# Performance work log

Hardware: AMD Instinct MI355X
Metric: run time of the kernel (lower is better)

## Reference

```python
import jax, jax.numpy as jnp
import numpy as np

N_QUBIT = 14
N_LAYER = 16
BATCH = 512
DIM = 2 ** N_QUBIT

# wire 0 is the most-significant bit (deepquantum convention: state.reshape([2]*n), wire i = axis i)
_bits = (np.arange(DIM)[:, None] >> (N_QUBIT - 1 - np.arange(N_QUBIT))) & 1
SIGNS = jnp.asarray(2.0 * _bits - 1.0, dtype=jnp.float32)  # (DIM, n_qubit), -1 for bit=0, +1 for bit=1


def _apply_1q(state, gate, w):
    # state: (B, DIM) complex64; gate: (2,2) complex
    B = state.shape[0]
    left, right = 2 ** w, 2 ** (N_QUBIT - w - 1)
    st = state.reshape(B, left, 2, right)
    return jnp.einsum('ab,xlbr->xlar', gate, st).reshape(B, DIM)


def _cnot(state, c, t):
    # CNOT control c, target t: X on target where control bit = 1
    B = state.shape[0]
    st = state.reshape((B,) + (2,) * N_QUBIT)
    ax_c, ax_t = c + 1, t + 1
    a0 = jnp.take(st, 0, axis=ax_c)
    a1 = jnp.take(st, 1, axis=ax_c)
    a1 = jnp.flip(a1, axis=ax_t if ax_t < ax_c else ax_t - 1)  # flip size-2 axis == X gate
    return jnp.stack([a0, a1], axis=ax_c).reshape(B, DIM)


def _rz_layer(state, thetas):
    # RZ(th) = diag(e^{-i th/2}, e^{+i th/2}) on every wire -> single fused diagonal phase
    return state * jnp.exp(0.5j * (SIGNS @ thetas))


def _ry_layer(state, thetas):
    for w in range(N_QUBIT):
        c = jnp.cos(thetas[w] * 0.5)
        s = jnp.sin(thetas[w] * 0.5)
        gate = jnp.stack([jnp.stack([c, -s]), jnp.stack([s, c])]).astype(jnp.complex64)
        state = _apply_1q(state, gate, w)
    return state


def _circuit(z, theta):
    state = z.reshape(z.shape[0], DIM)
    for l in range(N_LAYER):
        state = _rz_layer(state, theta[l, 0])
        state = _ry_layer(state, theta[l, 1])
        state = _rz_layer(state, theta[l, 2])
        for w in range(N_QUBIT):  # cnot_ring
            state = _cnot(state, w, (w + 1) % N_QUBIT)
    return state


def _split(state, w):
    B = state.shape[0]
    st = state.reshape(B, 2 ** w, 2, 2 ** (N_QUBIT - w - 1))
    return st[:, :, 0, :], st[:, :, 1, :]


def _expectations(state):
    outs = []
    for w in (0, 1):  # <Z_w> = sum |psi_0|^2 - |psi_1|^2
        p0, p1 = _split(state, w)
        outs.append(jnp.sum(jnp.abs(p0) ** 2 - jnp.abs(p1) ** 2, axis=(1, 2)))
    cross0 = None
    for w in (0, 1):  # <X_w> = 2 Re sum conj(psi_0) psi_1
        p0, p1 = _split(state, w)
        cr = jnp.conj(p0) * p1
        if w == 0:
            cross0 = cr
        outs.append(2.0 * jnp.sum(jnp.real(cr), axis=(1, 2)))
    outs.append(2.0 * jnp.sum(jnp.imag(cross0), axis=(1, 2)))  # <Y_0> = 2 Im sum conj(psi_0) psi_1
    return jnp.stack(outs, axis=1).astype(jnp.float32)  # (B, 5)


def setup_inputs() -> dict:
    key = jax.random.key(0)
    k1, k2, k3, k4 = jax.random.split(key, 4)
    zr = jax.random.normal(k1, (BATCH, DIM), dtype=jnp.float32)
    zi = jax.random.normal(k2, (BATCH, DIM), dtype=jnp.float32)
    z = (zr + 1j * zi).astype(jnp.complex64)
    z = z / jnp.linalg.norm(z, axis=1, keepdims=True)  # normalized quantum states
    z = z[:, :, None]  # (B, 2^n, 1) per docstring
    theta = jax.random.normal(k3, (N_LAYER, 3, N_QUBIT), dtype=jnp.float32)
    y = jax.random.randint(k4, (BATCH,), 0, 5)
    return {"z": z, "theta": theta, "y": y}


def reference(z, theta, y):
    state = _circuit(z, theta)
    output = _expectations(state)
    logp = jax.nn.log_softmax(output, axis=1)
    loss = -jnp.mean(jnp.take_along_axis(logp, y[:, None], axis=1))
    return (loss, output)
```

## Files before the change

### kernel.cpp

```cpp
#include <hip/hip_runtime.h>
#include <hip/hip_bf16.h>

#define NQ     14
#define DIM    16384
#define NLAYER 16
#define BATCH  512
#define NT     1024

typedef float v2f __attribute__((ext_vector_type(2)));

__device__ __forceinline__ constexpr int POSB(int x){ return (x ^ ((x >> 5) & 31)) << 3; }

__device__ __forceinline__ float bf2f(unsigned int u16){
  union { unsigned int i; float f; } v; v.i = u16 << 16; return v.f;
}

__device__ __forceinline__ float thv(const void* th, int i, bool b16){
  return b16 ? bf2f(((const unsigned short*)th)[i]) : ((const float*)th)[i];
}

__device__ int srcF(int x){
  int v = x;
  #pragma unroll
  for (int k = 13; k >= 0; --k){
    int tb = 13 - ((k + 1) % 14);
    v ^= ((v >> (13 - k)) & 1) << tb;
  }
  return v;
}

__device__ __forceinline__ v2f cmul(v2f a, v2f b){
  v2f t, d;
  asm("v_pk_mul_f32 %0, %1, %2 op_sel:[0,0] op_sel_hi:[1,0]"
      : "=v"(t) : "v"(a), "v"(b));
  asm("v_pk_fma_f32 %0, %1, %2, %3 op_sel:[1,1,0] op_sel_hi:[0,1,1] neg_lo:[0,1,0]"
      : "=v"(d) : "v"(a), "v"(b), "v"(t));
  return d;
}

__device__ __forceinline__ void rot2(v2f& a0, v2f& a1, float c, float s){
  v2f c2 = (v2f){c, c}, s2 = (v2f){s, s};
  v2f t0 = a0;
  a0 = a0 * c2 - a1 * s2;
  a1 = t0 * s2 + a1 * c2;
}

__global__ __launch_bounds__(NT) __attribute__((amdgpu_waves_per_eu(4, 4)))
void qnn_circuit(const void* __restrict__ zraw,
                 const void* __restrict__ theta,
                 float* __restrict__ out)
{
  __shared__ v2f   S[DIM];
  __shared__ v2f   ph0H[128], ph0L[128], ph2H[128], ph2Lt[128];
  __shared__ float csT[28];
  __shared__ int   sHB[128], sLB[128];
  __shared__ float red[16*5];

  char* Sb = (char*)S;
  const int t = threadIdx.x;
  const int b = blockIdx.x;

  int pred = 0;
  if (t < 336){
    unsigned int w  = ((const unsigned int*)theta)[t];
    unsigned int lo = w & 0xffffu;
    unsigned int e  = (lo >> 7) & 0xffu;
    pred = (e >= 100 && e <= 140) || (lo == 0);
  }
  const bool th_b16 = (__syncthreads_count(pred) > 250);

  pred = 0;
  if (t < 256){
    unsigned int w  = ((const unsigned int*)zraw)[t];
    unsigned int lo = w & 0xffffu;
    unsigned int e  = (lo >> 7) & 0xffu;
    pred = (e >= 88 && e <= 140) || (lo == 0);
  }
  const bool z_b16 = (__syncthreads_count(pred) > 160);

  if (t < 128){ sHB[t] = POSB(srcF(t << 7)); sLB[t] = POSB(srcF(t)); }

  if (z_b16){
    const uint4* zb = (const uint4*)((const unsigned short*)zraw + (size_t)b * (DIM * 2));
    #pragma unroll 1
    for (int jj = 0; jj < 4; ++jj){
      int x4 = t + NT * jj;
      uint4 w = zb[x4];
      int xb = x4 * 4;
      *(v2f*)(Sb + POSB(xb+0)) = (v2f){bf2f(w.x & 0xffffu), bf2f(w.x >> 16)};
      *(v2f*)(Sb + POSB(xb+1)) = (v2f){bf2f(w.y & 0xffffu), bf2f(w.y >> 16)};
      *(v2f*)(Sb + POSB(xb+2)) = (v2f){bf2f(w.z & 0xffffu), bf2f(w.z >> 16)};
      *(v2f*)(Sb + POSB(xb+3)) = (v2f){bf2f(w.w & 0xffffu), bf2f(w.w >> 16)};
    }
  } else {
    const float4* zf = (const float4*)((const float*)zraw + (size_t)b * DIM);
    #pragma unroll 1
    for (int jj = 0; jj < 4; ++jj){
      int x4 = t + NT * jj;
      float4 w = zf[x4];
      int xb = x4 * 4;
      *(v2f*)(Sb + POSB(xb+0)) = (v2f){w.x, 0.f};
      *(v2f*)(Sb + POSB(xb+1)) = (v2f){w.y, 0.f};
      *(v2f*)(Sb + POSB(xb+2)) = (v2f){w.z, 0.f};
      *(v2f*)(Sb + POSB(xb+3)) = (v2f){w.w, 0.f};
    }
  }
  __syncthreads();

  const int pwb = POSB(t);
  const int hb  = t >> 7;
  const int slB = sLB[t & 127];

  const int wv  = t >> 6, L = t & 63;
  const int pbA  = POSB((wv << 10) | L);
  const int pbB1 = POSB((wv << 10) | ((L >> 2) << 6) | (L & 3));
  const int pbB2 = POSB((wv << 10) | (L << 2));
  const int hB2  = (wv << 3) | (L >> 5);
  const int rB2  = L & 31;

  for (int l = 0; l < NLAYER; ++l){
    const int thb = l * 42;

    if (t < 512){
      int grp = t >> 7, idx = t & 127;
      int tz = thb + ((grp >= 2) ? 28 : 0);
      float ph = 0.f;
      if ((grp & 1) == 0){
        #pragma unroll
        for (int w = 0; w < 7; ++w)
          ph += (((idx >> (6 - w)) & 1) ? 0.5f : -0.5f) * thv(theta, tz + w, th_b16);
      } else {
        #pragma unroll
        for (int w = 7; w < 14; ++w)
          ph += (((idx >> (13 - w)) & 1) ? 0.5f : -0.5f) * thv(theta, tz + w, th_b16);
      }
      float sn, cs; sincosf(ph, &sn, &cs);
      v2f v = (v2f){cs, sn};
      if      (grp == 0) ph0H[idx] = v;
      else if (grp == 1) ph0L[idx] = v;
      else if (grp == 2) ph2H[idx] = v;
      else               ph2Lt[((idx & 3) << 5) | (idx >> 2)] = v;
    } else if (t < 512 + 14){
      int q = t - 512;
      float sn, cs; sincosf(0.5f * thv(theta, thb + 14 + q, th_b16), &sn, &cs);
      csT[2*q] = cs; csT[2*q+1] = sn;
    }

    {
      v2f g[16];
      if (l == 0){
        #pragma unroll
        for (int j = 0; j < 16; ++j) g[j] = *(v2f*)(Sb + (pwb ^ (j << 13)));
      } else {
        #pragma unroll
        for (int j = 0; j < 16; ++j)
          g[j] = *(v2f*)(Sb + (sHB[hb + 8*j] ^ slB));
      }
      __syncthreads();

      {
        v2f cl = ph0L[t & 127];
        #pragma unroll
        for (int j = 0; j < 16; ++j)
          g[j] = cmul(g[j], cmul(ph0H[hb + 8*j], cl));
      }
      #pragma unroll
      for (int q = 0; q < 4; ++q){
        float c = csT[2*q], sn = csT[2*q+1];
        int m = 8 >> q;
        #pragma unroll
        for (int j = 0; j < 16; ++j){
          if (j & m) continue;
          rot2(g[j], g[j | m], c, sn);
        }
      }
      #pragma unroll
      for (int j = 0; j < 16; ++j) *(v2f*)(Sb + (pwb ^ (j << 13))) = g[j];
    }
    __syncthreads();

    {
      v2f h[16];
      #pragma unroll
      for (int j = 0; j < 16; ++j) h[j] = *(v2f*)(Sb + (pbA ^ ((j << 9) | (j << 4))));
      #pragma unroll
      for (int q = 0; q < 4; ++q){
        float c = csT[2*(4+q)], sn = csT[2*(4+q)+1];
        int m = 8 >> q;
        #pragma unroll
        for (int j = 0; j < 16; ++j){
          if (j & m) continue;
          rot2(h[j], h[j | m], c, sn);
        }
      }
      #pragma unroll
      for (int j = 0; j < 16; ++j) *(v2f*)(Sb + (pbA ^ ((j << 9) | (j << 4)))) = h[j];
    }
    __threadfence_block();

    {
      v2f h[16];
      #pragma unroll
      for (int j = 0; j < 16; ++j)
        h[j] = *(v2f*)(Sb + (pbB1 ^ ((j << 5) ^ ((j >> 3) << 3))));
      #pragma unroll
      for (int q = 0; q < 4; ++q){
        float c = csT[2*(8+q)], sn = csT[2*(8+q)+1];
        int m = 8 >> q;
        #pragma unroll
        for (int j = 0; j < 16; ++j){
          if (j & m) continue;
          rot2(h[j], h[j | m], c, sn);
        }
      }
      #pragma unroll
      for (int j = 0; j < 16; ++j)
        *(v2f*)(Sb + (pbB1 ^ ((j << 5) ^ ((j >> 3) << 3)))) = h[j];
    }
    __threadfence_block();

    {
      v2f h[16];
      #pragma unroll
      for (int i = 0; i < 4; ++i){
        int gb = pbB2 ^ ((i << 11) | (i << 6));
        #pragma unroll
        for (int j = 0; j < 4; ++j) h[i*4+j] = *(v2f*)(Sb + (gb ^ (j << 3)));
      }
      #pragma unroll
      for (int q = 0; q < 2; ++q){
        float c = csT[2*(12+q)], sn = csT[2*(12+q)+1];
        int m = 2 >> q;
        #pragma unroll
        for (int r = 0; r < 16; ++r){
          if ((r & 3) & m) continue;
          rot2(h[r], h[r | m], c, sn);
        }
      }
      #pragma unroll
      for (int i = 0; i < 4; ++i){
        v2f chh = ph2H[hB2 | (i << 1)];
        #pragma unroll
        for (int j = 0; j < 4; ++j)
          h[i*4+j] = cmul(h[i*4+j], cmul(chh, ph2Lt[(j << 5) | rB2]));
      }
      #pragma unroll
      for (int i = 0; i < 4; ++i){
        int gb = pbB2 ^ ((i << 11) | (i << 6));
        #pragma unroll
        for (int j = 0; j < 4; ++j) *(v2f*)(Sb + (gb ^ (j << 3))) = h[i*4+j];
      }
    }
    __syncthreads();
  }

  float z0=0.f, z1=0.f, x0s=0.f, x1s=0.f, y0s=0.f;
  {
    v2f g[16];
    #pragma unroll
    for (int j = 0; j < 16; ++j)
      g[j] = *(v2f*)(Sb + (sHB[hb + 8*j] ^ slB));

    #pragma unroll
    for (int j = 0; j < 16; ++j){
      float pw = g[j].x*g[j].x + g[j].y*g[j].y;
      z0 += (j & 8) ? -pw : pw;
      z1 += (j & 4) ? -pw : pw;
    }
    #pragma unroll
    for (int j = 0; j < 8; ++j){
      v2f p0 = g[j], p1 = g[j+8];
      x0s += 2.f*(p0.x*p1.x + p0.y*p1.y);
      y0s += 2.f*(p0.x*p1.y - p0.y*p1.x);
    }
    #pragma unroll
    for (int j = 0; j < 16; ++j){
      if (j & 4) continue;
      v2f p0 = g[j], p1 = g[j|4];
      x1s += 2.f*(p0.x*p1.x + p0.y*p1.y);
    }
  }
  #pragma unroll
  for (int o = 32; o >= 1; o >>= 1){
    z0  += __shfl_down(z0,  o, 64);
    z1  += __shfl_down(z1,  o, 64);
    x0s += __shfl_down(x0s, o, 64);
    x1s += __shfl_down(x1s, o, 64);
    y0s += __shfl_down(y0s, o, 64);
  }
  int wid = t >> 6, lane = t & 63;
  if (lane == 0){
    red[wid*5+0]=z0; red[wid*5+1]=z1; red[wid*5+2]=x0s; red[wid*5+3]=x1s; red[wid*5+4]=y0s;
  }
  __syncthreads();
  if (t < 5){
    float sum = 0.f;
    #pragma unroll
    for (int w = 0; w < 16; ++w) sum += red[w*5 + t];
    out[1 + b*5 + t] = sum;
  }
}

__global__ __launch_bounds__(512)
void qnn_loss(const int* __restrict__ y, float* __restrict__ out)
{
  __shared__ float red[8];
  int t = threadIdx.x;
  const float* o = out + 1 + t*5;
  float o0=o[0], o1=o[1], o2=o[2], o3=o[3], o4=o[4];
  float m = fmaxf(fmaxf(fmaxf(o0,o1), fmaxf(o2,o3)), o4);
  float sum = expf(o0-m)+expf(o1-m)+expf(o2-m)+expf(o3-m)+expf(o4-m);
  float lse = m + logf(sum);
  int yi = y[t]; yi = yi < 0 ? 0 : (yi > 4 ? 4 : yi);
  float lb = lse - o[yi];

  #pragma unroll
  for (int ofs = 32; ofs >= 1; ofs >>= 1) lb += __shfl_down(lb, ofs, 64);
  if ((t & 63) == 0) red[t >> 6] = lb;
  __syncthreads();
  if (t == 0){
    float s = 0.f;
    #pragma unroll
    for (int w = 0; w < 8; ++w) s += red[w];
    out[0] = s / (float)BATCH;
  }
}

extern "C" void kernel_launch(void* const* d_in, const int* in_sizes, int n_in,
                              void* d_out, int out_size, void* d_ws, size_t ws_size,
                              hipStream_t stream)
{
  const void* z     = d_in[0];
  const void* theta = d_in[1];
  const int*  y     = (const int*)d_in[2];
  float*      out   = (float*)d_out;

  qnn_circuit<<<BATCH, NT, 0, stream>>>(z, theta, out);
  qnn_loss<<<1, 512, 0, stream>>>(y, out);
}
```

Before: 264.3 us.

## Apply last two RY wires via DPP lane swaps and fold the pass away

The RY rotations on wires 12 and 13 now run inside the earlier LDS pass, which holds 4..7 in registers, with their partners fetched from neighbouring lanes by DPP quad permutes and combined using per-lane signs. The second RZ phase is moved into the following pass, with a re-permuted phase table indexed for that pass's layout. This removes one full read-modify-write of the 16K-entry shared state per layer, along with a block fence. In exchange it adds cross-lane permute instructions and relies on the lane-to-bit mapping being correct.

```diff
diff --git a/kernel.cpp b/kernel.cpp
--- a/kernel.cpp
+++ b/kernel.cpp
@@ -45,13 +45,23 @@
   a1 = t0 * s2 + a1 * c2;
 }
 
+template<int CTRL>
+__device__ __forceinline__ v2f quad_swap(v2f a){
+  union { float f; int i; } xl, xh;
+  xl.f = a.x; xh.f = a.y;
+  union { int i; float f; } rl, rh;
+  rl.i = __builtin_amdgcn_mov_dpp(xl.i, CTRL, 0xf, 0xf, true);
+  rh.i = __builtin_amdgcn_mov_dpp(xh.i, CTRL, 0xf, 0xf, true);
+  return (v2f){rl.f, rh.f};
+}
+
 __global__ __launch_bounds__(NT) __attribute__((amdgpu_waves_per_eu(4, 4)))
 void qnn_circuit(const void* __restrict__ zraw,
                  const void* __restrict__ theta,
                  float* __restrict__ out)
 {
   __shared__ v2f   S[DIM];
-  __shared__ v2f   ph0H[128], ph0L[128], ph2H[128], ph2Lt[128];
+  __shared__ v2f   ph0H[128], ph0L[128], ph2Ht[128], ph2Lt[128];
   __shared__ float csT[28];
   __shared__ int   sHB[128], sLB[128];
   __shared__ float red[16*5];
@@ -114,9 +124,10 @@
   const int wv  = t >> 6, L = t & 63;
   const int pbA  = POSB((wv << 10) | L);
   const int pbB1 = POSB((wv << 10) | ((L >> 2) << 6) | (L & 3));
-  const int pbB2 = POSB((wv << 10) | (L << 2));
-  const int hB2  = (wv << 3) | (L >> 5);
-  const int rB2  = L & 31;
+  const int hB1  = (wv << 3) | (L >> 3);
+  const int lB1  = L & 7;
+  const float sg0 = (t & 1) ? 1.f : -1.f;
+  const float sg1 = (t & 2) ? 1.f : -1.f;
 
   for (int l = 0; l < NLAYER; ++l){
     const int thb = l * 42;
@@ -138,8 +149,8 @@
       v2f v = (v2f){cs, sn};
       if      (grp == 0) ph0H[idx] = v;
       else if (grp == 1) ph0L[idx] = v;
-      else if (grp == 2) ph2H[idx] = v;
-      else               ph2Lt[((idx & 3) << 5) | (idx >> 2)] = v;
+      else if (grp == 2) ph2Ht[idx] = v;
+      else               ph2Lt[(idx & 3) | (((idx >> 6) & 1) << 2) | (((idx >> 2) & 15) << 3)] = v;
     } else if (t < 512 + 14){
       int q = t - 512;
       float sn, cs; sincosf(0.5f * thv(theta, thb + 14 + q, th_b16), &sn, &cs);
@@ -193,6 +204,24 @@
           rot2(h[j], h[j | m], c, sn);
         }
       }
+      {
+        float c13 = csT[26], s13 = csT[27];
+        v2f c13v = (v2f){c13, c13};
+        v2f s13v = (v2f){sg0 * s13, sg0 * s13};
+        #pragma unroll
+        for (int j = 0; j < 16; ++j){
+          v2f p = quad_swap<0xB1>(h[j]);
+          h[j] = h[j] * c13v + p * s13v;
+        }
+        float c12 = csT[24], s12 = csT[25];
+        v2f c12v = (v2f){c12, c12};
+        v2f s12v = (v2f){sg1 * s12, sg1 * s12};
+        #pragma unroll
+        for (int j = 0; j < 16; ++j){
+          v2f p = quad_swap<0x4E>(h[j]);
+          h[j] = h[j] * c12v + p * s12v;
+        }
+      }
       #pragma unroll
       for (int j = 0; j < 16; ++j) *(v2f*)(Sb + (pbA ^ ((j << 9) | (j << 4)))) = h[j];
     }
@@ -213,43 +242,15 @@
           rot2(h[j], h[j | m], c, sn);
         }
       }
+      {
+        v2f chh = ph2Ht[hB1];
+        #pragma unroll
+        for (int j = 0; j < 16; ++j)
+          h[j] = cmul(h[j], cmul(chh, ph2Lt[lB1 | (j << 3)]));
+      }
       #pragma unroll
       for (int j = 0; j < 16; ++j)
         *(v2f*)(Sb + (pbB1 ^ ((j << 5) ^ ((j >> 3) << 3)))) = h[j];
-    }
-    __threadfence_block();
-
-    {
-      v2f h[16];
-      #pragma unroll
-      for (int i = 0; i < 4; ++i){
-        int gb = pbB2 ^ ((i << 11) | (i << 6));
-        #pragma unroll
-        for (int j = 0; j < 4; ++j) h[i*4+j] = *(v2f*)(Sb + (gb ^ (j << 3)));
-      }
-      #pragma unroll
-      for (int q = 0; q < 2; ++q){
-        float c = csT[2*(12+q)], sn = csT[2*(12+q)+1];
-        int m = 2 >> q;
-        #pragma unroll
-        for (int r = 0; r < 16; ++r){
-          if ((r & 3) & m) continue;
-          rot2(h[r], h[r | m], c, sn);
-        }
-      }
-      #pragma unroll
-      for (int i = 0; i < 4; ++i){
-        v2f chh = ph2H[hB2 | (i << 1)];
-        #pragma unroll
-        for (int j = 0; j < 4; ++j)
-          h[i*4+j] = cmul(h[i*4+j], cmul(chh, ph2Lt[(j << 5) | rB2]));
-      }
-      #pragma unroll
-      for (int i = 0; i < 4; ++i){
-        int gb = pbB2 ^ ((i << 11) | (i << 6));
-        #pragma unroll
-        for (int j = 0; j < 4; ++j) *(v2f*)(Sb + (gb ^ (j << 3))) = h[i*4+j];
-      }
     }
     __syncthreads();
   }
```

Result: faster. 253.3 us (-4.2%).
